# Optimization experiments

Measured on AMD Instinct MI355X. Metric: run time of the kernel, lower is better.

Reference implementation:

```python
import jax, jax.numpy as jnp
import numpy as np

EPS = 0.3
LAYER_NUM = 2
N_NODES = 50000
N_EDGES = 1600000
IN_CH = 256
HIDDEN = 128
OUT_CH = 64


def setup_inputs() -> dict:
    key = jax.random.key(0)
    ks = jax.random.split(key, 8)
    x = jax.random.normal(ks[0], (N_NODES, IN_CH), dtype=jnp.float32)
    edge_index = jax.random.randint(ks[1], (2, N_EDGES), 0, N_NODES, dtype=jnp.int64)
    # xavier-normal-ish scales
    t1_w = jax.random.normal(ks[2], (HIDDEN, IN_CH), dtype=jnp.float32) * (1.414 * (2.0 / (IN_CH + HIDDEN)) ** 0.5)
    t1_b = jnp.zeros((HIDDEN,), dtype=jnp.float32)
    gate_w = jax.random.normal(ks[3], (LAYER_NUM, 2 * HIDDEN), dtype=jnp.float32) * ((2.0 / (2 * HIDDEN + 1)) ** 0.5)
    gate_b = jnp.zeros((LAYER_NUM,), dtype=jnp.float32)
    t2_w = jax.random.normal(ks[4], (OUT_CH, HIDDEN), dtype=jnp.float32) * (1.414 * (2.0 / (HIDDEN + OUT_CH)) ** 0.5)
    t2_b = jnp.zeros((OUT_CH,), dtype=jnp.float32)
    return {"x": x, "edge_index": edge_index, "t1_w": t1_w, "t1_b": t1_b,
            "gate_w": gate_w, "gate_b": gate_b, "t2_w": t2_w, "t2_b": t2_b}


def reference(x, edge_index, t1_w, t1_b, gate_w, gate_b, t2_w, t2_b):
    n = x.shape[0]
    row, col = edge_index[0], edge_index[1]
    # symmetric degree normalization: deg computed over target nodes (row)
    deg = jax.ops.segment_sum(jnp.ones_like(row, dtype=x.dtype), row, num_segments=n)
    dinv = jnp.where(deg > 0, jax.lax.rsqrt(jnp.maximum(deg, 1.0)), 0.0)  # [N]
    edge_norm = dinv[row] * dinv[col]  # [E]

    h = jax.nn.relu(x @ t1_w.T + t1_b)  # [N, H]
    raw = h
    H = h.shape[1]
    for l in range(LAYER_NUM):
        gw_i = gate_w[l, :H]   # weights for h_src (row)
        gw_j = gate_w[l, H:]   # weights for h_dst (col)
        # edge attention g = tanh(gate([h_row || h_col]))  -> [E]
        g = jnp.tanh(h[row] @ gw_i + h[col] @ gw_j + gate_b[l])
        w = g * edge_norm  # [E]
        # scatter-add weighted neighbor features to target nodes
        agg = jax.ops.segment_sum(w[:, None] * h[col], row, num_segments=n)  # [N, H]
        h = EPS * raw + agg
    out = h @ t2_w.T + t2_b  # [N, out]
    return jax.nn.log_softmax(out, axis=1)
```

## Files before the change

kernel.cpp:

```cpp
#include <hip/hip_runtime.h>
#include <math.h>

#define EPSF 0.3f
#define NPB 128
#define SHB 7
#define MAXNB 512
#define CHUNK 4096
#define MAXSEG 8192

typedef __attribute__((ext_vector_type(8))) short bf16x8;
typedef __attribute__((ext_vector_type(4))) float f32x4;

__device__ __forceinline__ uint32_t f2bf(float f) {
    uint32_t u = __float_as_uint(f);
    return (u + 0x7fffu + ((u >> 16) & 1u)) >> 16;
}
__device__ __forceinline__ uint32_t pack2(float lo, float hi) {
    return f2bf(lo) | (f2bf(hi) << 16);
}
__device__ __forceinline__ float bflo(uint32_t u) { return __uint_as_float(u << 16); }
__device__ __forceinline__ float bfhi(uint32_t u) { return __uint_as_float(u & 0xffff0000u); }

__device__ __forceinline__ float fast_tanh(float x) {
    float e = __expf(2.f * x);
    return 1.f - 2.f * __builtin_amdgcn_rcpf(e + 1.f);
}

__device__ __forceinline__ int edge_at(const int* ei, int is64, size_t idx) {
    if (is64) return (int)((const long long*)ei)[idx];
    return ei[idx];
}

__device__ __forceinline__ int detect_is64(const int* ei, int base, int E) {
    __shared__ int s_nz;
    if (threadIdx.x == 0) s_nz = 0;
    __syncthreads();
    int lim = min(512, E - base);
    int nz = 0;
    for (int t = threadIdx.x; t < lim; t += 256)
        nz |= (ei[2 * (size_t)(base + t) + 1] != 0);
    if (nz) atomicOr(&s_nz, 1);
    __syncthreads();
    return s_nz == 0;
}

__device__ __forceinline__ void scan512(int* s) {
    int t = threadIdx.x;
    for (int o = 1; o < MAXNB; o <<= 1) {
        int i2 = t + 256;
        int x1 = (t >= o) ? s[t - o] : 0;
        int x2 = (i2 >= o) ? s[i2 - o] : 0;
        __syncthreads();
        s[t] += x1;
        s[i2] += x2;
        __syncthreads();
    }
}

__global__ __launch_bounds__(256) void k_pack(const int* __restrict__ ei, int E,
                                              uint32_t* __restrict__ pk,
                                              int* __restrict__ hist, int nblk, int NB) {
    __shared__ int lh[MAXNB];
    int base = blockIdx.x * CHUNK;
    int is64 = detect_is64(ei, base, E);
    for (int b = threadIdx.x; b < NB; b += 256) lh[b] = 0;
    __syncthreads();
    for (int j = threadIdx.x; j < CHUNK; j += 256) {
        int e = base + j;
        if (e < E) {
            int r = edge_at(ei, is64, e);
            int c = edge_at(ei, is64, (size_t)E + e);
            pk[e] = ((uint32_t)r << 16) | (uint32_t)c;
            atomicAdd(&lh[r >> SHB], 1);
        }
    }
    __syncthreads();
    for (int b = threadIdx.x; b < NB; b += 256)
        hist[(size_t)b * nblk + blockIdx.x] = lh[b];
}

__global__ void k_scanA(int* __restrict__ hist, int nblk, int* __restrict__ btot) {
    int b = blockIdx.x;
    int lane = threadIdx.x;
    int run = 0;
    for (int seg = 0; seg < nblk; seg += 64) {
        int idx = seg + lane;
        int v = (idx < nblk) ? hist[(size_t)b * nblk + idx] : 0;
        int s = v;
        for (int o = 1; o < 64; o <<= 1) {
            int t = __shfl_up(s, o);
            if (lane >= o) s += t;
        }
        if (idx < nblk) hist[(size_t)b * nblk + idx] = run + s - v;
        run += __shfl(s, 63);
    }
    if (lane == 0) btot[b] = run;
}

__global__ __launch_bounds__(256) void k_binwrite(const uint32_t* __restrict__ pk, int E,
                                                  const int* __restrict__ hist,
                                                  const int* __restrict__ btot,
                                                  uint32_t* __restrict__ ebuf,
                                                  int nblk, int NB) {
    __shared__ int s[MAXNB];
    __shared__ int lcnt[MAXNB];
    int t = threadIdx.x;
    for (int b = t; b < MAXNB; b += 256) s[b] = (b < NB) ? btot[b] : 0;
    __syncthreads();
    scan512(s);
    for (int b = t; b < NB; b += 256)
        lcnt[b] = s[b] - btot[b] + hist[(size_t)b * nblk + blockIdx.x];
    __syncthreads();
    int base = blockIdx.x * CHUNK;
    for (int j = t; j < CHUNK; j += 256) {
        int e = base + j;
        if (e < E) {
            uint32_t v = __builtin_nontemporal_load(&pk[e]);
            int pos = atomicAdd(&lcnt[v >> (16 + SHB)], 1);
            ebuf[pos] = v;
        }
    }
}

__global__ __launch_bounds__(256) void k_csr(const uint32_t* __restrict__ ebuf,
                                             const int* __restrict__ btot,
                                             int* __restrict__ rp, float* __restrict__ dinv,
                                             int* __restrict__ ecol, int N, int E, int NB) {
    __shared__ int s[MAXNB];
    __shared__ uint32_t seg[MAXSEG];
    __shared__ int cnt[NPB];
    __shared__ int sc[NPB];
    __shared__ int cur[NPB];
    int b = blockIdx.x;
    int tid = threadIdx.x;
    for (int k = tid; k < MAXNB; k += 256) s[k] = (k < NB) ? btot[k] : 0;
    __syncthreads();
    scan512(s);
    int p1 = s[b];
    int p0 = p1 - btot[b];
    int len = p1 - p0;
    bool fits = (len <= MAXSEG);
    int n0 = b << SHB;
    if (tid < NPB) cnt[tid] = 0;
    __syncthreads();
    if (fits) {
        for (int j = tid; j < len; j += 256) {
            uint32_t v = ebuf[p0 + j];
            seg[j] = v;
            atomicAdd(&cnt[(v >> 16) & (NPB - 1)], 1);
        }
    } else {
        for (int j = tid; j < len; j += 256)
            atomicAdd(&cnt[(ebuf[p0 + j] >> 16) & (NPB - 1)], 1);
    }
    __syncthreads();
    if (tid < NPB) sc[tid] = cnt[tid];
    __syncthreads();
    for (int o = 1; o < NPB; o <<= 1) {
        int v = (tid < NPB && tid >= o) ? sc[tid - o] : 0;
        __syncthreads();
        if (tid < NPB) sc[tid] += v;
        __syncthreads();
    }
    if (tid < NPB) {
        int off = sc[tid] - cnt[tid];
        cur[tid] = off;
        int node = n0 + tid;
        if (node < N) {
            rp[node] = p0 + off;
            int d = cnt[tid];
            dinv[node] = d > 0 ? rsqrtf((float)d) : 0.f;
        }
    }
    if (b == NB - 1 && tid == 0) rp[N] = E;
    __syncthreads();
    if (fits) {
        for (int j = tid; j < len; j += 256) {
            uint32_t v = seg[j];
            int pos = p0 + atomicAdd(&cur[(v >> 16) & (NPB - 1)], 1);
            ecol[pos] = (int)(v & 0xffffu);
        }
    } else {
        for (int j = tid; j < len; j += 256) {
            uint32_t v = ebuf[p0 + j];
            int pos = p0 + atomicAdd(&cur[(v >> 16) & (NPB - 1)], 1);
            ecol[pos] = (int)(v & 0xffffu);
        }
    }
}

__global__ __launch_bounds__(256) void k_gemm1(const float* __restrict__ A,
                                               const float* __restrict__ W,
                                               const float* __restrict__ bias,
                                               uint32_t* __restrict__ hb,
                                               const float* __restrict__ gw0,
                                               const float* __restrict__ gb,
                                               const float* __restrict__ dinv,
                                               float* __restrict__ av,
                                               float2* __restrict__ bd, int M) {
    __shared__ char As[128 * 128];
    __shared__ char Bs[128 * 128];
    __shared__ float pab_a[2][128];
    __shared__ float pab_b[2][128];
    const int tid = threadIdx.x;
    const int lane = tid & 63;
    const int wave = tid >> 6;
    const int wr = wave >> 1, wc = wave & 1;
    const int m0 = blockIdx.x * 128;
    const int lrow = lane & 15, lkg = lane >> 4;
    const int sr = tid >> 3;
    const int sc = (tid & 7) * 8;

    f32x4 acc[4][4];
#pragma unroll
    for (int mi = 0; mi < 4; ++mi)
#pragma unroll
        for (int ni = 0; ni < 4; ++ni) acc[mi][ni] = (f32x4){0.f, 0.f, 0.f, 0.f};

    for (int t = 0; t < 4; ++t) {
        const int k0 = t * 64;
#pragma unroll
        for (int i = 0; i < 4; ++i) {
            int r = i * 32 + sr;
            float4 v0 = make_float4(0.f, 0.f, 0.f, 0.f), v1 = v0;
            if (m0 + r < M) {
                const float* p = &A[(size_t)(m0 + r) * 256 + k0 + sc];
                v0 = *(const float4*)p;
                v1 = *(const float4*)(p + 4);
            }
            uint4 pk = make_uint4(pack2(v0.x, v0.y), pack2(v0.z, v0.w),
                                  pack2(v1.x, v1.y), pack2(v1.z, v1.w));
            uint32_t off = (uint32_t)(r * 128 + sc * 2);
            *(uint4*)(As + (off ^ ((r & 7) << 4))) = pk;
        }
#pragma unroll
        for (int i = 0; i < 4; ++i) {
            int r = i * 32 + sr;
            const float* p = &W[(size_t)r * 256 + k0 + sc];
            float4 v0 = *(const float4*)p;
            float4 v1 = *(const float4*)(p + 4);
            uint4 pk = make_uint4(pack2(v0.x, v0.y), pack2(v0.z, v0.w),
                                  pack2(v1.x, v1.y), pack2(v1.z, v1.w));
            uint32_t off = (uint32_t)(r * 128 + sc * 2);
            *(uint4*)(Bs + (off ^ ((r & 7) << 4))) = pk;
        }
        __syncthreads();
#pragma unroll
        for (int ks = 0; ks < 2; ++ks) {
            bf16x8 af[4], bfr[4];
#pragma unroll
            for (int mi = 0; mi < 4; ++mi) {
                int r = wr * 64 + mi * 16 + lrow;
                uint32_t off = (uint32_t)(r * 128 + ks * 64 + lkg * 16);
                af[mi] = *(const bf16x8*)(As + (off ^ ((r & 7) << 4)));
            }
#pragma unroll
            for (int ni = 0; ni < 4; ++ni) {
                int r = wc * 64 + ni * 16 + lrow;
                uint32_t off = (uint32_t)(r * 128 + ks * 64 + lkg * 16);
                bfr[ni] = *(const bf16x8*)(Bs + (off ^ ((r & 7) << 4)));
            }
#pragma unroll
            for (int mi = 0; mi < 4; ++mi)
#pragma unroll
                for (int ni = 0; ni < 4; ++ni)
                    acc[mi][ni] = __builtin_amdgcn_mfma_f32_16x16x32_bf16(
                        af[mi], bfr[ni], acc[mi][ni], 0, 0, 0);
        }
        __syncthreads();
    }
    float bv[4], gi[4], gj[4];
#pragma unroll
    for (int ni = 0; ni < 4; ++ni) {
        int n = wc * 64 + ni * 16 + lrow;
        bv[ni] = bias[n];
        gi[ni] = gw0[n];
        gj[ni] = gw0[128 + n];
    }
#pragma unroll
    for (int mi = 0; mi < 4; ++mi) {
#pragma unroll
        for (int q = 0; q < 4; ++q) {
            float pa = 0.f, pb = 0.f;
            int m = m0 + wr * 64 + mi * 16 + lkg * 4 + q;
#pragma unroll
            for (int ni = 0; ni < 4; ++ni) {
                float v = fmaxf(acc[mi][ni][q] + bv[ni], 0.f);
                float vp = __shfl_xor(v, 1);
                if (!(lane & 1) && m < M) {
                    int n = wc * 64 + ni * 16 + lrow;
                    hb[(size_t)m * 64 + (n >> 1)] = pack2(v, vp);
                }
                pa = fmaf(v, gi[ni], pa);
                pb = fmaf(v, gj[ni], pb);
            }
#pragma unroll
            for (int o = 1; o < 16; o <<= 1) {
                pa += __shfl_xor(pa, o);
                pb += __shfl_xor(pb, o);
            }
            if (lrow == 0) {
                int rl = wr * 64 + mi * 16 + lkg * 4 + q;
                pab_a[wc][rl] = pa;
                pab_b[wc][rl] = pb;
            }
        }
    }
    __syncthreads();
    if (tid < 128) {
        int m = m0 + tid;
        if (m < M) {
            av[m] = pab_a[0][tid] + pab_a[1][tid] + gb[0];
            bd[m] = make_float2(pab_b[0][tid] + pab_b[1][tid], dinv[m]);
        }
    }
}

__global__ __launch_bounds__(256) void k_gemm2(const uint32_t* __restrict__ Abf,
                                               const float* __restrict__ W,
                                               const float* __restrict__ bias,
                                               float* __restrict__ out, int M) {
    __shared__ char As[128 * 128];
    __shared__ char Bs[64 * 128];
    __shared__ float redmax[2][128];
    __shared__ float redsum[2][128];
    const int tid = threadIdx.x;
    const int lane = tid & 63;
    const int wave = tid >> 6;
    const int wr = wave >> 1, wc = wave & 1;
    const int m0 = blockIdx.x * 128;
    const int lrow = lane & 15, lkg = lane >> 4;

    f32x4 acc[4][2];
#pragma unroll
    for (int mi = 0; mi < 4; ++mi)
#pragma unroll
        for (int ni = 0; ni < 2; ++ni) acc[mi][ni] = (f32x4){0.f, 0.f, 0.f, 0.f};

    for (int t = 0; t < 2; ++t) {
#pragma unroll
        for (int i = 0; i < 4; ++i) {
            int r = i * 32 + (tid >> 3);
            uint4 v = make_uint4(0u, 0u, 0u, 0u);
            if (m0 + r < M)
                v = *(const uint4*)&Abf[(size_t)(m0 + r) * 64 + t * 32 + (tid & 7) * 4];
            uint32_t off = (uint32_t)(r * 128 + (tid & 7) * 16);
            *(uint4*)(As + (off ^ ((r & 7) << 4))) = v;
        }
#pragma unroll
        for (int i = 0; i < 2; ++i) {
            int r = i * 32 + (tid >> 3);
            const float* p = &W[(size_t)r * 128 + t * 64 + (tid & 7) * 8];
            float4 v0 = *(const float4*)p, v1 = *(const float4*)(p + 4);
            uint4 pk = make_uint4(pack2(v0.x, v0.y), pack2(v0.z, v0.w),
                                  pack2(v1.x, v1.y), pack2(v1.z, v1.w));
            uint32_t off = (uint32_t)(r * 128 + (tid & 7) * 16);
            *(uint4*)(Bs + (off ^ ((r & 7) << 4))) = pk;
        }
        __syncthreads();
#pragma unroll
        for (int ks = 0; ks < 2; ++ks) {
            bf16x8 af[4], bfr[2];
#pragma unroll
            for (int mi = 0; mi < 4; ++mi) {
                int r = wr * 64 + mi * 16 + lrow;
                uint32_t off = (uint32_t)(r * 128 + ks * 64 + lkg * 16);
                af[mi] = *(const bf16x8*)(As + (off ^ ((r & 7) << 4)));
            }
#pragma unroll
            for (int ni = 0; ni < 2; ++ni) {
                int r = wc * 32 + ni * 16 + lrow;
                uint32_t off = (uint32_t)(r * 128 + ks * 64 + lkg * 16);
                bfr[ni] = *(const bf16x8*)(Bs + (off ^ ((r & 7) << 4)));
            }
#pragma unroll
            for (int mi = 0; mi < 4; ++mi)
#pragma unroll
                for (int ni = 0; ni < 2; ++ni)
                    acc[mi][ni] = __builtin_amdgcn_mfma_f32_16x16x32_bf16(
                        af[mi], bfr[ni], acc[mi][ni], 0, 0, 0);
        }
        __syncthreads();
    }

    float vb[4][2][4];
#pragma unroll
    for (int mi = 0; mi < 4; ++mi)
#pragma unroll
        for (int ni = 0; ni < 2; ++ni) {
            float bvx = bias[wc * 32 + ni * 16 + lrow];
#pragma unroll
            for (int q = 0; q < 4; ++q) vb[mi][ni][q] = acc[mi][ni][q] + bvx;
        }
#pragma unroll
    for (int mi = 0; mi < 4; ++mi)
#pragma unroll
        for (int q = 0; q < 4; ++q) {
            float mx = fmaxf(vb[mi][0][q], vb[mi][1][q]);
#pragma unroll
            for (int o = 1; o < 16; o <<= 1) mx = fmaxf(mx, __shfl_xor(mx, o));
            if (lrow == 0) redmax[wc][wr * 64 + mi * 16 + lkg * 4 + q] = mx;
        }
    __syncthreads();
    float fmv[4][4];
#pragma unroll
    for (int mi = 0; mi < 4; ++mi)
#pragma unroll
        for (int q = 0; q < 4; ++q) {
            int rl = wr * 64 + mi * 16 + lkg * 4 + q;
            float fm = fmaxf(redmax[0][rl], redmax[1][rl]);
            fmv[mi][q] = fm;
            float e = expf(vb[mi][0][q] - fm) + expf(vb[mi][1][q] - fm);
#pragma unroll
            for (int o = 1; o < 16; o <<= 1) e += __shfl_xor(e, o);
            if (lrow == 0) redsum[wc][rl] = e;
        }
    __syncthreads();
#pragma unroll
    for (int mi = 0; mi < 4; ++mi)
#pragma unroll
        for (int q = 0; q < 4; ++q) {
            int rl = wr * 64 + mi * 16 + lkg * 4 + q;
            int m = m0 + rl;
            if (m < M) {
                float ls = logf(redsum[0][rl] + redsum[1][rl]) + fmv[mi][q];
                out[(size_t)m * 64 + wc * 32 + lrow] = vb[mi][0][q] - ls;
                out[(size_t)m * 64 + wc * 32 + 16 + lrow] = vb[mi][1][q] - ls;
            }
        }
}

template <bool FUSE_AB, bool RAW_NT>
__global__ __launch_bounds__(256) void k_agg(const uint32_t* __restrict__ hb,
                                             const uint32_t* __restrict__ raw,
                                             const int* __restrict__ rp,
                                             const int* __restrict__ ecol,
                                             const float* __restrict__ av,
                                             const float2* __restrict__ bd,
                                             const float* __restrict__ dinv,
                                             uint32_t* __restrict__ hb_out,
                                             const float* __restrict__ gw_next,
                                             const float* __restrict__ gb_next,
                                             float* __restrict__ av_out,
                                             float2* __restrict__ bd_out, int N) {
    int wid = threadIdx.x >> 6, lane = threadIdx.x & 63;
    int i = blockIdx.x * 4 + wid;
    if (i >= N) return;
    int iu = __builtin_amdgcn_readfirstlane(i);
    int p0 = __builtin_amdgcn_readfirstlane(rp[iu]);
    int p1 = __builtin_amdgcn_readfirstlane(rp[iu + 1]);
    float a_i = av[iu];
    float di = dinv[iu];
    const int lg = lane >> 4;
    const int ll = lane & 15;
    const char* hbp = (const char*)hb + (ll << 4);

    uint32_t r0 = 0, r1 = 0, r2 = 0, r3 = 0;
    if (lane < 16) {
        const uint32_t* rpt = raw + (size_t)i * 64 + ll * 4;
        if (RAW_NT) {
            r0 = __builtin_nontemporal_load(rpt + 0);
            r1 = __builtin_nontemporal_load(rpt + 1);
            r2 = __builtin_nontemporal_load(rpt + 2);
            r3 = __builtin_nontemporal_load(rpt + 3);
        } else {
            r0 = rpt[0]; r1 = rpt[1]; r2 = rpt[2]; r3 = rpt[3];
        }
    }

    float acc[8];
#pragma unroll
    for (int j = 0; j < 8; ++j) acc[j] = 0.f;

#define FMA8(W, U)                                                              \
    acc[0] = fmaf(W, bflo((U).x), acc[0]); acc[1] = fmaf(W, bfhi((U).x), acc[1]); \
    acc[2] = fmaf(W, bflo((U).y), acc[2]); acc[3] = fmaf(W, bfhi((U).y), acc[3]); \
    acc[4] = fmaf(W, bflo((U).z), acc[4]); acc[5] = fmaf(W, bfhi((U).z), acc[5]); \
    acc[6] = fmaf(W, bflo((U).w), acc[6]); acc[7] = fmaf(W, bfhi((U).w), acc[7]);

    for (int b0 = p0; b0 < p1; b0 += 64) {
        int cnt = min(64, p1 - b0);
        uint32_t wcp = 0u;
        if (lane < cnt) {
            int c = __builtin_nontemporal_load(&ecol[b0 + lane]);
            float2 t = bd[c];
            float w = fast_tanh(a_i + t.x) * t.y;
            wcp = (f2bf(w) << 16) | (uint32_t)c;
        }
        int cntp = (cnt + 15) & ~15;
        for (int k = 0; k < cntp; k += 16) {
            int kb = (k + lg) << 2;
            uint32_t wx0 = __builtin_amdgcn_ds_bpermute(kb, (int)wcp);
            uint32_t wx1 = __builtin_amdgcn_ds_bpermute(kb + 16, (int)wcp);
            uint32_t wx2 = __builtin_amdgcn_ds_bpermute(kb + 32, (int)wcp);
            uint32_t wx3 = __builtin_amdgcn_ds_bpermute(kb + 48, (int)wcp);
            uint4 u0 = *(const uint4*)(hbp + ((wx0 & 0xffffu) << 8));
            uint4 u1 = *(const uint4*)(hbp + ((wx1 & 0xffffu) << 8));
            uint4 u2 = *(const uint4*)(hbp + ((wx2 & 0xffffu) << 8));
            uint4 u3 = *(const uint4*)(hbp + ((wx3 & 0xffffu) << 8));
            float w0 = bfhi(wx0), w1 = bfhi(wx1), w2 = bfhi(wx2), w3 = bfhi(wx3);
            FMA8(w0, u0);
            FMA8(w1, u1);
            FMA8(w2, u2);
            FMA8(w3, u3);
        }
    }
#undef FMA8
#pragma unroll
    for (int j = 0; j < 8; ++j) {
        acc[j] += __shfl_xor(acc[j], 16);
        acc[j] += __shfl_xor(acc[j], 32);
    }
    if (lane < 16) {
        float o[8];
        o[0] = EPSF * bflo(r0) + di * acc[0]; o[1] = EPSF * bfhi(r0) + di * acc[1];
        o[2] = EPSF * bflo(r1) + di * acc[2]; o[3] = EPSF * bfhi(r1) + di * acc[3];
        o[4] = EPSF * bflo(r2) + di * acc[4]; o[5] = EPSF * bfhi(r2) + di * acc[5];
        o[6] = EPSF * bflo(r3) + di * acc[6]; o[7] = EPSF * bfhi(r3) + di * acc[7];
        uint4 w4;
        w4.x = pack2(o[0], o[1]); w4.y = pack2(o[2], o[3]);
        w4.z = pack2(o[4], o[5]); w4.w = pack2(o[6], o[7]);
        *((uint4*)(hb_out + (size_t)i * 64) + ll) = w4;
        if (FUSE_AB) {
            float pa = 0.f, pb = 0.f;
#pragma unroll
            for (int j = 0; j < 8; ++j) {
                int ch = ll * 8 + j;
                pa = fmaf(o[j], gw_next[ch], pa);
                pb = fmaf(o[j], gw_next[128 + ch], pb);
            }
#pragma unroll
            for (int off = 1; off < 16; off <<= 1) {
                pa += __shfl_xor(pa, off);
                pb += __shfl_xor(pb, off);
            }
            if (ll == 0) {
                av_out[i] = pa + gb_next[0];
                bd_out[i] = make_float2(pb, di);
            }
        }
    }
}

extern "C" void kernel_launch(void* const* d_in, const int* in_sizes, int n_in,
                              void* d_out, int out_size, void* d_ws, size_t ws_size,
                              hipStream_t stream) {
    const float* x = (const float*)d_in[0];
    const int* ei = (const int*)d_in[1];
    const float* t1w = (const float*)d_in[2];
    const float* t1b = (const float*)d_in[3];
    const float* gw = (const float*)d_in[4];
    const float* gb = (const float*)d_in[5];
    const float* t2w = (const float*)d_in[6];
    const float* t2b = (const float*)d_in[7];
    float* out = (float*)d_out;

    const int INC = 256;
    const int N = in_sizes[0] / INC;
    const int E = in_sizes[1] / 2;
    const int NB = (N + NPB - 1) >> SHB;
    const int nblk = (E + CHUNK - 1) / CHUNK;

    char* ws = (char*)d_ws;
    auto alloc = [&](size_t bytes) {
        char* p = ws;
        ws += (bytes + 255) & ~(size_t)255;
        return p;
    };
    uint32_t* pk = (uint32_t*)alloc((size_t)E * 4);
    int* hist = (int*)alloc((size_t)NB * nblk * 4);
    int* btot = (int*)alloc((size_t)NB * 4);
    uint32_t* ebuf = (uint32_t*)alloc((size_t)E * 4);
    int* rp = (int*)alloc((size_t)(N + 1) * 4);
    float* dinv = (float*)alloc((size_t)N * 4);
    int* ecol = (int*)alloc((size_t)E * 4);
    float* av0 = (float*)alloc((size_t)N * 4);
    float* av1 = (float*)alloc((size_t)N * 4);
    float2* bd0 = (float2*)alloc((size_t)N * 8);
    float2* bd1 = (float2*)alloc((size_t)N * 8);
    uint32_t* hb0 = (uint32_t*)alloc((size_t)N * 64 * 4);
    uint32_t* hb1 = (uint32_t*)alloc((size_t)N * 64 * 4);
    uint32_t* hb2 = (uint32_t*)alloc((size_t)N * 64 * 4);

    k_pack<<<nblk, 256, 0, stream>>>(ei, E, pk, hist, nblk, NB);
    k_scanA<<<NB, 64, 0, stream>>>(hist, nblk, btot);
    k_binwrite<<<nblk, 256, 0, stream>>>(pk, E, hist, btot, ebuf, nblk, NB);
    k_csr<<<NB, 256, 0, stream>>>(ebuf, btot, rp, dinv, ecol, N, E, NB);

    k_gemm1<<<(N + 127) / 128, 256, 0, stream>>>(x, t1w, t1b, hb0,
                                                 gw + 0 * 256, gb, dinv, av0, bd0, N);

    k_agg<true, false><<<(N + 3) / 4, 256, 0, stream>>>(
        hb0, hb0, rp, ecol, av0, bd0, dinv, hb1, gw + 1 * 256, gb + 1, av1, bd1, N);
    k_agg<false, true><<<(N + 3) / 4, 256, 0, stream>>>(
        hb1, hb0, rp, ecol, av1, bd1, dinv, hb2, nullptr, nullptr, nullptr, nullptr, N);

    k_gemm2<<<(N + 127) / 128, 256, 0, stream>>>(hb2, t2w, t2b, out, N);
}
```

Baseline: 189.6 us.

## Split hidden features into four column slabs and aggregate each slab separately

Stores the bf16 hidden matrix as four 32-channel slabs (slab-major, node-minor) and launches the aggregation kernel with a second grid dimension over slabs. Each slab's gather footprint is a quarter of the full matrix, which should improve L2/MALL hit rates for random neighbor reads. The cost is that the edge weights (tanh gate) and the CSR column indices are now computed and read four times. The fused gate projection for the next layer is moved into a separate small kernel.

```diff
diff --git a/kernel.cpp b/kernel.cpp
--- a/kernel.cpp
+++ b/kernel.cpp
@@ -289,7 +289,7 @@
                 float vp = __shfl_xor(v, 1);
                 if (!(lane & 1) && m < M) {
                     int n = wc * 64 + ni * 16 + lrow;
-                    hb[(size_t)m * 64 + (n >> 1)] = pack2(v, vp);
+                    hb[((size_t)(n >> 5) * M + m) * 16 + ((n & 31) >> 1)] = pack2(v, vp);
                 }
                 pa = fmaf(v, gi[ni], pa);
                 pb = fmaf(v, gj[ni], pb);
@@ -341,10 +341,12 @@
 #pragma unroll
         for (int i = 0; i < 4; ++i) {
             int r = i * 32 + (tid >> 3);
+            int q = tid & 7;
             uint4 v = make_uint4(0u, 0u, 0u, 0u);
             if (m0 + r < M)
-                v = *(const uint4*)&Abf[(size_t)(m0 + r) * 64 + t * 32 + (tid & 7) * 4];
-            uint32_t off = (uint32_t)(r * 128 + (tid & 7) * 16);
+                v = *(const uint4*)&Abf[((size_t)(2 * t + (q >> 2)) * M + (m0 + r)) * 16 +
+                                        (q & 3) * 4];
+            uint32_t off = (uint32_t)(r * 128 + q * 16);
             *(uint4*)(As + (off ^ ((r & 7) << 4))) = v;
         }
 #pragma unroll
@@ -430,7 +432,30 @@
         }
 }
 
-template <bool FUSE_AB, bool RAW_NT>
+__global__ void k_ab(const uint32_t* __restrict__ hbv, const float* __restrict__ gw,
+                     const float* __restrict__ gb, int layer,
+                     const float* __restrict__ dinv,
+                     float* __restrict__ av, float2* __restrict__ bd, int N) {
+    int wid = threadIdx.x >> 6, lane = threadIdx.x & 63;
+    int i = blockIdx.x * 4 + wid;
+    if (i >= N) return;
+    uint32_t u = hbv[((size_t)(lane >> 4) * N + i) * 16 + (lane & 15)];
+    float hx = bflo(u), hy = bfhi(u);
+    float2 wi = *(const float2*)&gw[lane * 2];
+    float2 wj = *(const float2*)&gw[128 + lane * 2];
+    float pa = hx * wi.x + hy * wi.y;
+    float pb = hx * wj.x + hy * wj.y;
+    for (int o = 1; o < 64; o <<= 1) {
+        pa += __shfl_xor(pa, o);
+        pb += __shfl_xor(pb, o);
+    }
+    if (lane == 0) {
+        av[i] = pa + gb[layer];
+        bd[i] = make_float2(pb, dinv[i]);
+    }
+}
+
+template <bool RAW_NT>
 __global__ __launch_bounds__(256) void k_agg(const uint32_t* __restrict__ hb,
                                              const uint32_t* __restrict__ raw,
                                              const int* __restrict__ rp,
@@ -438,11 +463,8 @@
                                              const float* __restrict__ av,
                                              const float2* __restrict__ bd,
                                              const float* __restrict__ dinv,
-                                             uint32_t* __restrict__ hb_out,
-                                             const float* __restrict__ gw_next,
-                                             const float* __restrict__ gb_next,
-                                             float* __restrict__ av_out,
-                                             float2* __restrict__ bd_out, int N) {
+                                             uint32_t* __restrict__ hb_out, int N) {
+    const int pass = blockIdx.y;
     int wid = threadIdx.x >> 6, lane = threadIdx.x & 63;
     int i = blockIdx.x * 4 + wid;
     if (i >= N) return;
@@ -451,20 +473,20 @@
     int p1 = __builtin_amdgcn_readfirstlane(rp[iu + 1]);
     float a_i = av[iu];
     float di = dinv[iu];
-    const int lg = lane >> 4;
-    const int ll = lane & 15;
-    const char* hbp = (const char*)hb + (ll << 4);
-
-    uint32_t r0 = 0, r1 = 0, r2 = 0, r3 = 0;
-    if (lane < 16) {
-        const uint32_t* rpt = raw + (size_t)i * 64 + ll * 4;
+    const int lg = lane >> 2;
+    const int ll = lane & 3;
+    const char* hbp = (const char*)(hb + (size_t)pass * N * 16) + (ll << 4);
+
+    uint32_t ru0 = 0, ru1 = 0, ru2 = 0, ru3 = 0;
+    if (lane < 4) {
+        const uint32_t* rpt = raw + ((size_t)pass * N + i) * 16 + lane * 4;
         if (RAW_NT) {
-            r0 = __builtin_nontemporal_load(rpt + 0);
-            r1 = __builtin_nontemporal_load(rpt + 1);
-            r2 = __builtin_nontemporal_load(rpt + 2);
-            r3 = __builtin_nontemporal_load(rpt + 3);
+            ru0 = __builtin_nontemporal_load(rpt + 0);
+            ru1 = __builtin_nontemporal_load(rpt + 1);
+            ru2 = __builtin_nontemporal_load(rpt + 2);
+            ru3 = __builtin_nontemporal_load(rpt + 3);
         } else {
-            r0 = rpt[0]; r1 = rpt[1]; r2 = rpt[2]; r3 = rpt[3];
+            ru0 = rpt[0]; ru1 = rpt[1]; ru2 = rpt[2]; ru3 = rpt[3];
         }
     }
 
@@ -487,58 +509,36 @@
             float w = fast_tanh(a_i + t.x) * t.y;
             wcp = (f2bf(w) << 16) | (uint32_t)c;
         }
-        int cntp = (cnt + 15) & ~15;
-        for (int k = 0; k < cntp; k += 16) {
+        int cntp = (cnt + 31) & ~31;
+        for (int k = 0; k < cntp; k += 32) {
             int kb = (k + lg) << 2;
             uint32_t wx0 = __builtin_amdgcn_ds_bpermute(kb, (int)wcp);
-            uint32_t wx1 = __builtin_amdgcn_ds_bpermute(kb + 16, (int)wcp);
-            uint32_t wx2 = __builtin_amdgcn_ds_bpermute(kb + 32, (int)wcp);
-            uint32_t wx3 = __builtin_amdgcn_ds_bpermute(kb + 48, (int)wcp);
-            uint4 u0 = *(const uint4*)(hbp + ((wx0 & 0xffffu) << 8));
-            uint4 u1 = *(const uint4*)(hbp + ((wx1 & 0xffffu) << 8));
-            uint4 u2 = *(const uint4*)(hbp + ((wx2 & 0xffffu) << 8));
-            uint4 u3 = *(const uint4*)(hbp + ((wx3 & 0xffffu) << 8));
-            float w0 = bfhi(wx0), w1 = bfhi(wx1), w2 = bfhi(wx2), w3 = bfhi(wx3);
+            uint32_t wx1 = __builtin_amdgcn_ds_bpermute(kb + 64, (int)wcp);
+            uint4 u0 = *(const uint4*)(hbp + ((wx0 & 0xffffu) << 6));
+            uint4 u1 = *(const uint4*)(hbp + ((wx1 & 0xffffu) << 6));
+            float w0 = bfhi(wx0), w1 = bfhi(wx1);
             FMA8(w0, u0);
             FMA8(w1, u1);
-            FMA8(w2, u2);
-            FMA8(w3, u3);
         }
     }
 #undef FMA8
 #pragma unroll
     for (int j = 0; j < 8; ++j) {
+        acc[j] += __shfl_xor(acc[j], 4);
+        acc[j] += __shfl_xor(acc[j], 8);
         acc[j] += __shfl_xor(acc[j], 16);
         acc[j] += __shfl_xor(acc[j], 32);
     }
-    if (lane < 16) {
+    if (lane < 4) {
         float o[8];
-        o[0] = EPSF * bflo(r0) + di * acc[0]; o[1] = EPSF * bfhi(r0) + di * acc[1];
-        o[2] = EPSF * bflo(r1) + di * acc[2]; o[3] = EPSF * bfhi(r1) + di * acc[3];
-        o[4] = EPSF * bflo(r2) + di * acc[4]; o[5] = EPSF * bfhi(r2) + di * acc[5];
-        o[6] = EPSF * bflo(r3) + di * acc[6]; o[7] = EPSF * bfhi(r3) + di * acc[7];
+        o[0] = EPSF * bflo(ru0) + di * acc[0]; o[1] = EPSF * bfhi(ru0) + di * acc[1];
+        o[2] = EPSF * bflo(ru1) + di * acc[2]; o[3] = EPSF * bfhi(ru1) + di * acc[3];
+        o[4] = EPSF * bflo(ru2) + di * acc[4]; o[5] = EPSF * bfhi(ru2) + di * acc[5];
+        o[6] = EPSF * bflo(ru3) + di * acc[6]; o[7] = EPSF * bfhi(ru3) + di * acc[7];
         uint4 w4;
         w4.x = pack2(o[0], o[1]); w4.y = pack2(o[2], o[3]);
         w4.z = pack2(o[4], o[5]); w4.w = pack2(o[6], o[7]);
-        *((uint4*)(hb_out + (size_t)i * 64) + ll) = w4;
-        if (FUSE_AB) {
-            float pa = 0.f, pb = 0.f;
-#pragma unroll
-            for (int j = 0; j < 8; ++j) {
-                int ch = ll * 8 + j;
-                pa = fmaf(o[j], gw_next[ch], pa);
-                pb = fmaf(o[j], gw_next[128 + ch], pb);
-            }
-#pragma unroll
-            for (int off = 1; off < 16; off <<= 1) {
-                pa += __shfl_xor(pa, off);
-                pb += __shfl_xor(pb, off);
-            }
-            if (ll == 0) {
-                av_out[i] = pa + gb_next[0];
-                bd_out[i] = make_float2(pb, di);
-            }
-        }
+        *((uint4*)(hb_out + ((size_t)pass * N + i) * 16) + lane) = w4;
     }
 }
 
@@ -560,6 +560,7 @@
     const int E = in_sizes[1] / 2;
     const int NB = (N + NPB - 1) >> SHB;
     const int nblk = (E + CHUNK - 1) / CHUNK;
+    const int nbb = (N + 3) / 4;
 
     char* ws = (char*)d_ws;
     auto alloc = [&](size_t bytes) {
@@ -590,10 +591,11 @@
     k_gemm1<<<(N + 127) / 128, 256, 0, stream>>>(x, t1w, t1b, hb0,
                                                  gw + 0 * 256, gb, dinv, av0, bd0, N);
 
-    k_agg<true, false><<<(N + 3) / 4, 256, 0, stream>>>(
-        hb0, hb0, rp, ecol, av0, bd0, dinv, hb1, gw + 1 * 256, gb + 1, av1, bd1, N);
-    k_agg<false, true><<<(N + 3) / 4, 256, 0, stream>>>(
-        hb1, hb0, rp, ecol, av1, bd1, dinv, hb2, nullptr, nullptr, nullptr, nullptr, N);
+    k_agg<false><<<dim3(nbb, 4), 256, 0, stream>>>(
+        hb0, hb0, rp, ecol, av0, bd0, dinv, hb1, N);
+    k_ab<<<nbb, 256, 0, stream>>>(hb1, gw + 1 * 256, gb, 1, dinv, av1, bd1, N);
+    k_agg<true><<<dim3(nbb, 4), 256, 0, stream>>>(
+        hb1, hb0, rp, ecol, av1, bd1, dinv, hb2, N);
 
     k_gemm2<<<(N + 127) / 128, 256, 0, stream>>>(hb2, t2w, t2b, out, N);
 }
```

Measured after the change: 290.5 us. 1.53x slower.
